# Kernel tuning notes

Measured on AMD Instinct MI355X. Metric: run time of the kernel, lower is better.

## Reference

```python
import jax, jax.numpy as jnp
import numpy as np

B, S, X, Y = 32, 3, 512, 512  # batch, O(3) spin components, lattice X, lattice Y

_L_np = np.array([[[0, 0, 0], [0, 0, -1], [0, 1, 0]],
                  [[0, 0, 1], [0, 0, 0], [-1, 0, 0]],
                  [[0, -1, 0], [1, 0, 0], [0, 0, 0]]], dtype=np.float32)


def setup_inputs() -> dict:
    key = jax.random.key(0)
    k_s, = jax.random.split(key, 1)
    s = jax.random.normal(k_s, (B, S, X, Y), dtype=jnp.float32)
    t = jnp.ones((), dtype=jnp.float32)
    C0 = jnp.ones((), dtype=jnp.float32)  # cc=[1.0] learnable coefficient
    L = jnp.asarray(_L_np)                # fixed SO(3) generators [s, r, a]
    return {"s": s, "t": t, "C0": C0, "L": L}


def reference(s, t, C0, L):
    # Psi0.grad: F = sum_mu (roll(s,+1,mu) + roll(s,-1,mu)); nearest-neighbor stencil
    Fn = (jnp.roll(s, 1, axis=2) + jnp.roll(s, -1, axis=2)
          + jnp.roll(s, 1, axis=3) + jnp.roll(s, -1, axis=3))
    # Lsig = -einsum('bsxy,sra->braxy', s, L); out = einsum('bsaxy,bsxy->baxy', Lsig, Fn)
    # fused: out[b,a,x,y] = -sum_{s,r} s[b,s,x,y] * L[s,r,a] * Fn[b,r,x,y]
    F = -jnp.einsum('bsxy,sra,brxy->baxy', s, L, Fn)
    # Coeff(t): cc=[1.0], EvenOdd=True, single coeff => Coeff(t) = C0 (t-independent)
    coeff = C0
    return coeff * F
```

## Files before the change

kernel.cpp:

```cpp
#include <hip/hip_runtime.h>
#include <hip/hip_bf16.h>


constexpr int B = 32, X = 512, Y = 512;
constexpr int XY = X * Y;

__global__ __launch_bounds__(256)
void psi0_kernel(const float* __restrict__ s,
                 const float* __restrict__ C0p,
                 const float* __restrict__ Lp,
                 float* __restrict__ out)
{
    __shared__ float Ls[27];
    if (threadIdx.x < 27) Ls[threadIdx.x] = Lp[threadIdx.x];
    __syncthreads();

    const int tid = threadIdx.x;
    const int ty  = tid & 127;
    const int row = tid >> 7;
    const int bid = blockIdx.x;
    const int b   = bid >> 8;
    const int x   = ((bid & 255) << 1) + row;
    const int y0  = ty << 2;

    const int xm = (x == 0)     ? X - 1 : x - 1;
    const int xp = (x == X - 1) ? 0     : x + 1;
    const int ym = (y0 == 0)    ? Y - 1 : y0 - 1;
    const int yp = (y0 + 4 == Y) ? 0    : y0 + 4;

    const float C0 = C0p[0];
    const size_t baseB = (size_t)b * 3 * XY;

    float4 sc[3];
    float4 Fn[3];

    #pragma unroll
    for (int c = 0; c < 3; ++c) {
        const float* p = s + baseB + (size_t)c * XY;
        const float4 ce = *(const float4*)(p + (size_t)x  * Y + y0);
        const float4 up = *(const float4*)(p + (size_t)xm * Y + y0);
        const float4 dn = *(const float4*)(p + (size_t)xp * Y + y0);
        const float  lf = p[(size_t)x * Y + ym];
        const float  rt = p[(size_t)x * Y + yp];
        sc[c] = ce;
        Fn[c].x = up.x + dn.x + lf   + ce.y;
        Fn[c].y = up.y + dn.y + ce.x + ce.z;
        Fn[c].z = up.z + dn.z + ce.y + ce.w;
        Fn[c].w = up.w + dn.w + ce.z + rt;
    }

    #pragma unroll
    for (int a = 0; a < 3; ++a) {
        float4 acc = make_float4(0.f, 0.f, 0.f, 0.f);
        #pragma unroll
        for (int ss = 0; ss < 3; ++ss) {
            #pragma unroll
            for (int r = 0; r < 3; ++r) {
                const float w = Ls[ss * 9 + r * 3 + a];
                acc.x += w * sc[ss].x * Fn[r].x;
                acc.y += w * sc[ss].y * Fn[r].y;
                acc.z += w * sc[ss].z * Fn[r].z;
                acc.w += w * sc[ss].w * Fn[r].w;
            }
        }
        float4 o;
        o.x = -C0 * acc.x;
        o.y = -C0 * acc.y;
        o.z = -C0 * acc.z;
        o.w = -C0 * acc.w;
        *(float4*)(out + baseB + (size_t)a * XY + (size_t)x * Y + y0) = o;
    }
}

extern "C" void kernel_launch(void* const* d_in, const int* in_sizes, int n_in,
                              void* d_out, int out_size, void* d_ws, size_t ws_size,
                              hipStream_t stream)
{
    const float* s   = (const float*)d_in[0];
    const float* C0p = (const float*)d_in[2];
    const float* Lp  = (const float*)d_in[3];
    float* out = (float*)d_out;

    const int blocks = B * (X / 2);
    psi0_kernel<<<blocks, 256, 0, stream>>>(s, C0p, Lp, out);
}
```

Measured before the change: 182.6 us.

## Swizzle block order, shuffle horizontal halos, use nontemporal output stores

Remaps block indices so that consecutive blocks are spread across 8 groups, which changes how work lands on chiplets and caches. The left and right neighbour values now come from wavefront shuffles, and only the edge lanes issue scalar global loads. Output is written with nontemporal stores so results do not pollute the cache. The kernel is memory-bound, so any gain depends on cache and channel behaviour, and the swizzle could hurt L2 locality across neighbouring rows.

New measurement: 183.5 us. No clear change (+0.5%).

```diff
diff --git a/kernel.cpp b/kernel.cpp
--- a/kernel.cpp
+++ b/kernel.cpp
@@ -4,6 +4,8 @@
 
 constexpr int B = 32, X = 512, Y = 512;
 constexpr int XY = X * Y;
+
+typedef float v4f __attribute__((ext_vector_type(4)));
 
 __global__ __launch_bounds__(256)
 void psi0_kernel(const float* __restrict__ s,
@@ -15,60 +17,76 @@
     if (threadIdx.x < 27) Ls[threadIdx.x] = Lp[threadIdx.x];
     __syncthreads();
 
-    const int tid = threadIdx.x;
-    const int ty  = tid & 127;
-    const int row = tid >> 7;
-    const int bid = blockIdx.x;
-    const int b   = bid >> 8;
-    const int x   = ((bid & 255) << 1) + row;
-    const int y0  = ty << 2;
+    const int tid  = threadIdx.x;
+    const int lane = tid & 63;
+    const int ty   = tid & 127;
+    const int row  = tid >> 7;
+
+    const int per = gridDim.x >> 3;
+    const int sw  = (blockIdx.x & 7) * per + (blockIdx.x >> 3);
+
+    const int b  = sw >> 8;
+    const int x  = ((sw & 255) << 1) + row;
+    const int y0 = ty << 2;
 
     const int xm = (x == 0)     ? X - 1 : x - 1;
     const int xp = (x == X - 1) ? 0     : x + 1;
-    const int ym = (y0 == 0)    ? Y - 1 : y0 - 1;
-    const int yp = (y0 + 4 == Y) ? 0    : y0 + 4;
+    const int ym = (y0 == 0)     ? Y - 1 : y0 - 1;
+    const int yp = (y0 + 4 == Y) ? 0     : y0 + 4;
 
-    const float C0 = C0p[0];
     const size_t baseB = (size_t)b * 3 * XY;
+    const float* p0 = s + baseB;
+    const size_t rc = (size_t)x  * Y + y0;
+    const size_t ru = (size_t)xm * Y + y0;
+    const size_t rd = (size_t)xp * Y + y0;
 
-    float4 sc[3];
-    float4 Fn[3];
-
+    v4f ce[3], up[3], dn[3];
     #pragma unroll
     for (int c = 0; c < 3; ++c) {
-        const float* p = s + baseB + (size_t)c * XY;
-        const float4 ce = *(const float4*)(p + (size_t)x  * Y + y0);
-        const float4 up = *(const float4*)(p + (size_t)xm * Y + y0);
-        const float4 dn = *(const float4*)(p + (size_t)xp * Y + y0);
-        const float  lf = p[(size_t)x * Y + ym];
-        const float  rt = p[(size_t)x * Y + yp];
-        sc[c] = ce;
-        Fn[c].x = up.x + dn.x + lf   + ce.y;
-        Fn[c].y = up.y + dn.y + ce.x + ce.z;
-        Fn[c].z = up.z + dn.z + ce.y + ce.w;
-        Fn[c].w = up.w + dn.w + ce.z + rt;
+        const float* p = p0 + (size_t)c * XY;
+        ce[c] = *(const v4f*)(p + rc);
+        up[c] = *(const v4f*)(p + ru);
+        dn[c] = *(const v4f*)(p + rd);
     }
 
+    float lf[3], rt[3];
+    #pragma unroll
+    for (int c = 0; c < 3; ++c) {
+        lf[c] = __shfl_up(ce[c].w, 1);
+        rt[c] = __shfl_down(ce[c].x, 1);
+    }
+    if (lane == 0) {
+        #pragma unroll
+        for (int c = 0; c < 3; ++c) lf[c] = p0[(size_t)c * XY + (size_t)x * Y + ym];
+    }
+    if (lane == 63) {
+        #pragma unroll
+        for (int c = 0; c < 3; ++c) rt[c] = p0[(size_t)c * XY + (size_t)x * Y + yp];
+    }
+
+    v4f Fn[3];
+    #pragma unroll
+    for (int c = 0; c < 3; ++c) {
+        Fn[c].x = up[c].x + dn[c].x + lf[c]   + ce[c].y;
+        Fn[c].y = up[c].y + dn[c].y + ce[c].x + ce[c].z;
+        Fn[c].z = up[c].z + dn[c].z + ce[c].y + ce[c].w;
+        Fn[c].w = up[c].w + dn[c].w + ce[c].z + rt[c];
+    }
+
+    const float nC0 = -C0p[0];
     #pragma unroll
     for (int a = 0; a < 3; ++a) {
-        float4 acc = make_float4(0.f, 0.f, 0.f, 0.f);
+        v4f acc = (v4f)0.f;
         #pragma unroll
         for (int ss = 0; ss < 3; ++ss) {
             #pragma unroll
             for (int r = 0; r < 3; ++r) {
                 const float w = Ls[ss * 9 + r * 3 + a];
-                acc.x += w * sc[ss].x * Fn[r].x;
-                acc.y += w * sc[ss].y * Fn[r].y;
-                acc.z += w * sc[ss].z * Fn[r].z;
-                acc.w += w * sc[ss].w * Fn[r].w;
+                acc += w * ce[ss] * Fn[r];
             }
         }
-        float4 o;
-        o.x = -C0 * acc.x;
-        o.y = -C0 * acc.y;
-        o.z = -C0 * acc.z;
-        o.w = -C0 * acc.w;
-        *(float4*)(out + baseB + (size_t)a * XY + (size_t)x * Y + y0) = o;
+        v4f o = nC0 * acc;
+        __builtin_nontemporal_store(o, (v4f*)(out + baseB + (size_t)a * XY + rc));
     }
 }
 
```
